# Optimization experiments

Hardware: AMD Instinct MI355X
Metric: run time of the kernel (lower is better)

The kernel has to match this reference:

```python
import jax, jax.numpy as jnp
import numpy as np

K = 20
EPS = 1e-5
NEG_SLOPE = 0.2


def _bn(x, gamma, beta, axes):
    # batch-norm in training mode (batch statistics), per-channel on last axis
    mean = jnp.mean(x, axis=axes, keepdims=True)
    var = jnp.var(x, axis=axes, keepdims=True)
    return gamma * (x - mean) * jax.lax.rsqrt(var + EPS) + beta


def _lrelu(x):
    return jnp.where(x >= 0, x, NEG_SLOPE * x)


def setup_inputs() -> dict:
    key = jax.random.key(0)
    ks = jax.random.split(key, 8)
    B, C, N = 8, 6, 4096

    def w(k_, shape):
        fan_in = shape[-1]
        return jax.random.normal(k_, shape, jnp.float32) / np.sqrt(fan_in)

    return {
        "x": jax.random.normal(ks[0], (B, C, N), jnp.float32),
        "conv1_w": w(ks[1], (64, 12)),
        "bn1_g": jnp.ones((64,), jnp.float32), "bn1_b": jnp.zeros((64,), jnp.float32),
        "conv2_w": w(ks[2], (128, 64)),
        "bn2_g": jnp.ones((128,), jnp.float32), "bn2_b": jnp.zeros((128,), jnp.float32),
        "conv3_w": w(ks[3], (1024, 128)),
        "bn3_g": jnp.ones((1024,), jnp.float32), "bn3_b": jnp.zeros((1024,), jnp.float32),
        "fc1_w": w(ks[4], (512, 1024)),
        "bn4_g": jnp.ones((512,), jnp.float32), "bn4_b": jnp.zeros((512,), jnp.float32),
        "fc2_w": w(ks[5], (256, 512)),
        "bn5_g": jnp.ones((256,), jnp.float32), "bn5_b": jnp.zeros((256,), jnp.float32),
        "fc3_w": w(ks[6], (9, 256)), "fc3_b": jnp.zeros((9,), jnp.float32),
        "fc4_w": w(ks[7], (3, 256)), "fc4_b": jnp.zeros((3,), jnp.float32),
    }


def _get_graph_feature(x, k):
    # x: [B, C, N] -> [B, N, k, 2C]
    B, C, N = x.shape
    xt = jnp.transpose(x, (0, 2, 1))                      # [B, N, C]
    xx = jnp.sum(xt * xt, axis=-1)                        # [B, N]
    inner = jnp.einsum('bnc,bmc->bnm', xt, xt)            # [B, N, N]
    pd = 2.0 * inner - xx[:, :, None] - xx[:, None, :]    # -||xi-xj||^2
    _, idx = jax.lax.top_k(pd, k)                         # [B, N, k]
    nbr = xt[jnp.arange(B)[:, None, None], idx]           # [B, N, k, C]
    center = jnp.broadcast_to(xt[:, :, None, :], nbr.shape)
    return jnp.concatenate([nbr - center, center], axis=-1)  # [B, N, k, 2C]


def reference(x, conv1_w, bn1_g, bn1_b, conv2_w, bn2_g, bn2_b,
              conv3_w, bn3_g, bn3_b, fc1_w, bn4_g, bn4_b,
              fc2_w, bn5_g, bn5_b, fc3_w, fc3_b, fc4_w, fc4_b):
    B = x.shape[0]
    feat = _get_graph_feature(x, K)                            # [B, N, k, 12]
    h = _lrelu(_bn(jnp.einsum('bnkc,oc->bnko', feat, conv1_w), bn1_g, bn1_b, (0, 1, 2)))
    h = _lrelu(_bn(jnp.einsum('bnkc,oc->bnko', h, conv2_w), bn2_g, bn2_b, (0, 1, 2)))
    h = jnp.max(h, axis=2)                                     # [B, N, 128] max over k
    h = _lrelu(_bn(jnp.einsum('bnc,oc->bno', h, conv3_w), bn3_g, bn3_b, (0, 1)))
    g = jnp.max(h, axis=1)                                     # [B, 1024] max over points
    g = _lrelu(_bn(g @ fc1_w.T, bn4_g, bn4_b, (0,)))           # [B, 512]
    g = _lrelu(_bn(g @ fc2_w.T, bn5_g, bn5_b, (0,)))           # [B, 256]
    bias = (g @ fc4_w.T + fc4_b)[:, None, :]                   # [B, 1, 3]
    matrix = jnp.eye(3, dtype=x.dtype) + (g @ fc3_w.T + fc3_b).reshape(B, 3, 3)
    xyz = jnp.transpose(x[:, :3, :], (0, 2, 1))                # [B, N, 3]
    out = jnp.einsum('bnc,bcd->bnd', xyz, matrix) + bias       # [B, N, 3]
    return jnp.transpose(out, (0, 2, 1))                       # [B, 3, N]
```

## Files before the change

kernel.cpp:

```cpp
#include <hip/hip_runtime.h>
#include <math.h>
#include <stddef.h>


static constexpr float EPS_ = 1e-5f;

__global__ __launch_bounds__(256) void k_prep(const float* __restrict__ x,
                                              float* __restrict__ xtp,
                                              const float* __restrict__ w2,
                                              float* __restrict__ w2t)
{
    int i = blockIdx.x*256 + threadIdx.x;
    int b = i >> 12, n = i & 4095;
    const float* xb = x + (size_t)b*6*4096 + n;
    float v0 = xb[0], v1 = xb[4096], v2 = xb[2*4096];
    float v3 = xb[3*4096], v4 = xb[4*4096], v5 = xb[5*4096];
    float xx = v0*v0 + v1*v1 + v2*v2 + v3*v3 + v4*v4 + v5*v5;
    float4* o = (float4*)(xtp + (size_t)i*8);
    o[0] = make_float4(v0, v1, v2, v3);
    o[1] = make_float4(v4, v5, xx, 0.f);
    if (blockIdx.x < 2){
        int e = blockIdx.x*256 + threadIdx.x;
        for (int q = e; q < 64*128; q += 512){
            int c = q >> 7, oo = q & 127;
            w2t[q] = w2[oo*64 + c];
        }
    }
}

__device__ __forceinline__ float pd_calc(const float4 a0, const float4 a1,
                                         const float4 q0, const float4 q1)
{
    float dot = a0.x*q0.x;
    dot = fmaf(a0.y, q0.y, dot);
    dot = fmaf(a0.z, q0.z, dot);
    dot = fmaf(a0.w, q0.w, dot);
    dot = fmaf(a1.x, q1.x, dot);
    dot = fmaf(a1.y, q1.y, dot);
    return fmaf(2.f, dot, -a1.z - q1.z);
}

__device__ __forceinline__ unsigned fkey_(float f){
    unsigned u = __float_as_uint(f);
    return (u & 0x80000000u) ? ~u : (u | 0x80000000u);
}
__device__ __forceinline__ float finv_(unsigned k){
    return (k & 0x80000000u) ? __uint_as_float(k & 0x7fffffffu)
                             : __uint_as_float(~k);
}

#define TK_CAP 384
__global__ __launch_bounds__(256) void k_topk(const float* __restrict__ xtp,
                                              int* __restrict__ idxout)
{
    __shared__ float maxs[8][256];
    __shared__ float candv[4][TK_CAP];
    __shared__ int   candi[4][TK_CAP];
    __shared__ float Ts[8];
    __shared__ unsigned ccnt[4], ocnt[4], nwork;
    __shared__ unsigned short work[1024];

    const int t = threadIdx.x;
    const int rowbase = blockIdx.x << 3;
    const int b = rowbase >> 12;
    const float* xb = xtp + ((size_t)b << 15);

    float4 c0[8], c1[8];
    #pragma unroll
    for (int c = 0; c < 8; c++){
        const float4* p = (const float4*)(xtp + (size_t)(rowbase + c)*8);
        c0[c] = p[0]; c1[c] = p[1];
    }

    float mx[8];
    #pragma unroll
    for (int c = 0; c < 8; c++) mx[c] = -INFINITY;
    {
        const float4* qp = (const float4*)(xb + (size_t)t*8);
        for (int i = 0; i < 16; i++){
            float4 q0 = qp[0], q1 = qp[1];
            #pragma unroll
            for (int c = 0; c < 8; c++)
                mx[c] = fmaxf(mx[c], pd_calc(c0[c], c1[c], q0, q1));
            qp += 512;
        }
    }
    #pragma unroll
    for (int c = 0; c < 8; c++) maxs[c][t] = mx[c];
    __syncthreads();

    const int w = t >> 6, lane = t & 63;
    for (int cc = w; cc < 8; cc += 4){
        unsigned k0 = fkey_(maxs[cc][lane]);
        unsigned k1 = fkey_(maxs[cc][64  + lane]);
        unsigned k2 = fkey_(maxs[cc][128 + lane]);
        unsigned k3 = fkey_(maxs[cc][192 + lane]);
        unsigned lo = 0u;
        for (int bit = 31; bit >= 0; bit--){
            unsigned cand = lo | (1u << bit);
            int cnt = __popcll(__ballot(k0 >= cand))
                    + __popcll(__ballot(k1 >= cand))
                    + __popcll(__ballot(k2 >= cand))
                    + __popcll(__ballot(k3 >= cand));
            if (cnt >= 20) lo = cand;
        }
        if (lane == 0) Ts[cc] = finv_(lo);
    }
    __syncthreads();

    for (int p = 0; p < 2; p++){
        const int cb = p << 2;
        if (t < 4){ ccnt[t] = 0u; ocnt[t] = 0u; }
        if (t == 0) nwork = 0u;
        __syncthreads();

        #pragma unroll
        for (int c = 0; c < 4; c++){
            if (mx[cb + c] >= Ts[cb + c]){
                unsigned pos = atomicAdd(&nwork, 1u);
                work[pos] = (unsigned short)((c << 8) | t);
            }
        }
        __syncthreads();

        {
            int total = (int)nwork << 4;
            for (int e = t; e < total; e += 256){
                int ct = work[e >> 4];
                int c = ct >> 8, src = ct & 255;
                int m = ((e & 15) << 8) | src;
                const float4* pp = (const float4*)(xb + (size_t)m*8);
                float4 q0 = pp[0], q1 = pp[1];
                float pd = pd_calc(c0[cb + c], c1[cb + c], q0, q1);
                if (pd >= Ts[cb + c]){
                    unsigned pos = atomicAdd(&ccnt[c], 1u);
                    if (pos < TK_CAP){ candv[c][pos] = pd; candi[c][pos] = m; }
                }
            }
        }
        __syncthreads();

        {
            int n = (int)min(ccnt[w], (unsigned)TK_CAP);
            unsigned key[6]; int id[6];
            #pragma unroll
            for (int j = 0; j < 6; j++){
                int pz = (j << 6) | lane;
                bool ok = pz < n;
                key[j] = ok ? fkey_(candv[w][pz]) : 0u;
                id[j]  = ok ? candi[w][pz] : 0x7fffffff;
            }
            unsigned C = 0u;
            for (int bit = 31; bit >= 0; bit--){
                unsigned cand = C | (1u << bit);
                int cnt = 0;
                #pragma unroll
                for (int j = 0; j < 6; j++)
                    cnt += __popcll(__ballot(key[j] >= cand));
                if (cnt >= 20) C = cand;
            }
            int m = 0, e = 0;
            #pragma unroll
            for (int j = 0; j < 6; j++){
                m += __popcll(__ballot(key[j] > C));
                e += __popcll(__ballot(key[j] == C));
            }
            int* outp = idxout + (size_t)(rowbase + cb + w)*20;
            #pragma unroll
            for (int j = 0; j < 6; j++){
                if (key[j] > C){
                    unsigned pos = atomicAdd(&ocnt[w], 1u);
                    outp[pos] = id[j];
                }
            }
            int need = 20 - m;
            if (e <= need){
                #pragma unroll
                for (int j = 0; j < 6; j++){
                    if (key[j] == C){
                        unsigned pos = atomicAdd(&ocnt[w], 1u);
                        outp[pos] = id[j];
                    }
                }
            } else {
                for (int r = 0; r < need; r++){
                    int loc = 0x7fffffff;
                    #pragma unroll
                    for (int j = 0; j < 6; j++)
                        if (key[j] == C && id[j] < loc) loc = id[j];
                    int g = loc;
                    #pragma unroll
                    for (int s = 1; s < 64; s <<= 1) g = min(g, __shfl_xor(g, s));
                    #pragma unroll
                    for (int j = 0; j < 6; j++){
                        if (key[j] == C && id[j] == g){
                            key[j] = 0u;
                            unsigned pos = atomicAdd(&ocnt[w], 1u);
                            outp[pos] = g;
                        }
                    }
                }
            }
        }
        __syncthreads();
    }
}

__global__ __launch_bounds__(256) void k_bn1stats(const float* __restrict__ xtp,
                                                  const int* __restrict__ idxb,
                                                  const float* __restrict__ w1,
                                                  float* __restrict__ bn1sum,
                                                  float* __restrict__ bn1sq)
{
    __shared__ float fT[320*12];
    __shared__ float red[2][4][64];
    const int t = threadIdx.x;
    const int rowbase = blockIdx.x << 4;
    const int b = rowbase >> 12;

    for (int s = t; s < 320; s += 256){
        int r = s / 20, k = s % 20;
        int grow = rowbase + r;
        int m = idxb[(size_t)grow*20 + k];
        const float4* pn = (const float4*)(xtp + (size_t)((b << 12) | m)*8);
        const float4* pc = (const float4*)(xtp + (size_t)grow*8);
        float4 n0 = pn[0], n1 = pn[1], c0 = pc[0], c1 = pc[1];
        float* f = fT + s*12;
        ((float4*)f)[0] = make_float4(n0.x-c0.x, n0.y-c0.y, n0.z-c0.z, n0.w-c0.w);
        ((float4*)f)[1] = make_float4(n1.x-c1.x, n1.y-c1.y, c0.x, c0.y);
        ((float4*)f)[2] = make_float4(c0.z, c0.w, c1.x, c1.y);
    }
    __syncthreads();
    const int o = t & 63, grp = t >> 6;
    float w[12];
    #pragma unroll
    for (int c = 0; c < 12; c++) w[c] = w1[o*12 + c];
    float sm = 0.f, sq = 0.f;
    for (int s = grp*80; s < grp*80 + 80; s++){
        const float* f = fT + s*12;
        float4 f0 = *(const float4*)(f);
        float4 fa = *(const float4*)(f + 4);
        float4 fb = *(const float4*)(f + 8);
        float h = w[0]*f0.x + w[1]*f0.y + w[2]*f0.z + w[3]*f0.w
                + w[4]*fa.x + w[5]*fa.y + w[6]*fa.z + w[7]*fa.w
                + w[8]*fb.x + w[9]*fb.y + w[10]*fb.z + w[11]*fb.w;
        sm += h; sq = fmaf(h, h, sq);
    }
    red[0][grp][o] = sm; red[1][grp][o] = sq;
    __syncthreads();
    if (t < 64){
        float a = red[0][0][t] + red[0][1][t] + red[0][2][t] + red[0][3][t];
        float c2 = red[1][0][t] + red[1][1][t] + red[1][2][t] + red[1][3][t];
        atomicAdd(bn1sum + t, a);
        atomicAdd(bn1sq + t, c2);
    }
}

__global__ __launch_bounds__(256, 2) void k_conv12(
    const float* __restrict__ xtp, const int* __restrict__ idxb,
    const float* __restrict__ w1, const float* __restrict__ w2t,
    const float* __restrict__ bn1sum, const float* __restrict__ bn1sq,
    const float* __restrict__ bn1g, const float* __restrict__ bn1b,
    float* __restrict__ h2max, float* __restrict__ bn2sum, float* __restrict__ bn2sq)
{
    __shared__ float f1s[160*64];
    __shared__ float w2u[16*516];
    const int t = threadIdx.x;
    const int rowbase = blockIdx.x << 3;
    const int b = rowbase >> 12;

    const int jch = t & 63;
    float wr[12];
    #pragma unroll
    for (int c = 0; c < 12; c++) wr[c] = w1[jch*12 + c];
    float s1, t1;
    {
        float mean = bn1sum[jch]*(1.f/655360.f);
        float var  = bn1sq[jch]*(1.f/655360.f) - mean*mean;
        s1 = bn1g[jch]/sqrtf(var + EPS_);
        t1 = bn1b[jch] - mean*s1;
    }

    float* fT = w2u;
    if (t < 160){
        int r = t / 20;
        int grow = rowbase + r;
        int m = idxb[(size_t)grow*20 + (t - r*20)];
        const float4* pn = (const float4*)(xtp + (size_t)((b << 12) | m)*8);
        const float4* pc = (const float4*)(xtp + (size_t)grow*8);
        float4 n0 = pn[0], n1 = pn[1], c0 = pc[0], c1 = pc[1];
        float* f = fT + t*12;
        ((float4*)f)[0] = make_float4(n0.x-c0.x, n0.y-c0.y, n0.z-c0.z, n0.w-c0.w);
        ((float4*)f)[1] = make_float4(n1.x-c1.x, n1.y-c1.y, c0.x, c0.y);
        ((float4*)f)[2] = make_float4(c0.z, c0.w, c1.x, c1.y);
    }
    __syncthreads();
    {
        for (int vid = t; vid < 10240; vid += 256){
            int vec = vid >> 6;
            const float* f = fT + vec*12;
            float4 f0 = *(const float4*)(f);
            float4 fa = *(const float4*)(f + 4);
            float4 fb = *(const float4*)(f + 8);
            float acc = wr[0]*f0.x + wr[1]*f0.y + wr[2]*f0.z + wr[3]*f0.w
                      + wr[4]*fa.x + wr[5]*fa.y + wr[6]*fa.z + wr[7]*fa.w
                      + wr[8]*fb.x + wr[9]*fb.y + wr[10]*fb.z + wr[11]*fb.w;
            float v = fmaf(s1, acc, t1);
            int key = (((vec >> 2) ^ vec) & 7) << 2;
            f1s[(vec << 6) + (jch ^ key)] = fmaxf(v, 0.2f*v);
        }
    }
    __syncthreads();
    {
        float4 tmp[8];
        #pragma unroll
        for (int i = 0; i < 8; i++) tmp[i] = ((const float4*)w2t)[t + (i << 8)];
        #pragma unroll
        for (int i = 0; i < 8; i++){
            int q = t + (i << 8);
            int jr = q >> 5, o4 = q & 31;
            *(float4*)&w2u[(o4 >> 1)*516 + (jr << 3) + ((o4 & 1) << 2)] = tmp[i];
        }
    }
    __syncthreads();

    const int vg = t & 15, og = t >> 4;
    const float* fp = f1s + vg*10*64;
    const float* wp = w2u + og*516;
    int kw[10];
    #pragma unroll
    for (int i = 0; i < 10; i++){
        int vec = vg*10 + i;
        kw[i] = (((vec >> 2) ^ vec) & 7) << 2;
    }

    float h[10][8];
    #pragma unroll
    for (int i = 0; i < 10; i++)
        #pragma unroll
        for (int oi = 0; oi < 8; oi++) h[i][oi] = 0.f;

    for (int jl = 0; jl < 64; jl += 4){
        float wv[4][8];
        #pragma unroll
        for (int jj = 0; jj < 4; jj++){
            *(float4*)&wv[jj][0] = *(const float4*)&wp[((jl + jj) << 3)];
            *(float4*)&wv[jj][4] = *(const float4*)&wp[((jl + jj) << 3) + 4];
        }
        #pragma unroll
        for (int i = 0; i < 10; i++){
            float fv[4];
            *(float4*)fv = *(const float4*)&fp[(i << 6) + (jl ^ kw[i])];
            #pragma unroll
            for (int jj = 0; jj < 4; jj++)
                #pragma unroll
                for (int oi = 0; oi < 8; oi++)
                    h[i][oi] = fmaf(fv[jj], wv[jj][oi], h[i][oi]);
        }
    }

    float mxl[8], sml[8], sql[8];
    #pragma unroll
    for (int oi = 0; oi < 8; oi++){
        float v = h[0][oi];
        mxl[oi] = v; sml[oi] = v; sql[oi] = v*v;
    }
    #pragma unroll
    for (int i = 1; i < 10; i++)
        #pragma unroll
        for (int oi = 0; oi < 8; oi++){
            float v = h[i][oi];
            mxl[oi] = fmaxf(mxl[oi], v);
            sml[oi] += v;
            sql[oi] = fmaf(v, v, sql[oi]);
        }
    __syncthreads();
    {
        int base = vg*132 + (og << 3);
        *(float4*)&w2u[base]        = *(float4*)&mxl[0];
        *(float4*)&w2u[base + 4]    = *(float4*)&mxl[4];
        *(float4*)&w2u[2112 + base]     = *(float4*)&sml[0];
        *(float4*)&w2u[2112 + base + 4] = *(float4*)&sml[4];
        *(float4*)&w2u[4224 + base]     = *(float4*)&sql[0];
        *(float4*)&w2u[4224 + base + 4] = *(float4*)&sql[4];
    }
    __syncthreads();
    for (int it = t; it < 1024; it += 256){
        int r = it >> 7, o = it & 127;
        float m = fmaxf(w2u[(r << 1)*132 + o],
                        w2u[((r << 1) | 1)*132 + o]);
        h2max[(size_t)(rowbase + r)*128 + o] = m;
    }
    if (t < 128){
        float s = 0.f, qq = 0.f;
        #pragma unroll
        for (int u = 0; u < 16; u++){
            s  += w2u[2112 + u*132 + t];
            qq += w2u[4224 + u*132 + t];
        }
        atomicAdd(bn2sum + t, s);
        atomicAdd(bn2sq + t, qq);
    }
}

__global__ __launch_bounds__(256) void k_wt3(const float* __restrict__ w3,
                                             float* __restrict__ w3t)
{
    int i = blockIdx.x*256 + threadIdx.x;
    int j = i >> 10, o = i & 1023;
    w3t[i] = w3[(size_t)o*128 + j];
}

__global__ __launch_bounds__(256, 2) void k_conv3(const float* __restrict__ h2max,
    const float* __restrict__ bn2sum, const float* __restrict__ bn2sq,
    const float* __restrict__ bn2g, const float* __restrict__ bn2b,
    const float* __restrict__ w3t,
    float* __restrict__ bn3sum, float* __restrict__ bn3sq, unsigned int* __restrict__ gkey)
{
    __shared__ float f2[64*132];
    __shared__ float w3s[8192];
    __shared__ float bn2stL[256];
    const int t = threadIdx.x;
    const int bid = blockIdx.x;
    const int idx = bid >> 3;
    const int rt = (bid & 7)*64 + (idx >> 4);
    const int ot = idx & 15;
    const int rowbase = rt << 6;
    const int obase = ot << 6;
    const int b = rowbase >> 12;

    if (t < 128){
        float mean = bn2sum[t]*(1.f/655360.f);
        float var  = bn2sq[t]*(1.f/655360.f) - mean*mean;
        float s = bn2g[t]/sqrtf(var + EPS_);
        bn2stL[t] = s;
        bn2stL[128 + t] = bn2b[t] - mean*s;
    }
    __syncthreads();

    for (int e = t; e < 64*128; e += 256){
        int r = e >> 7, c = e & 127;
        float v = h2max[(size_t)(rowbase + r)*128 + c];
        float u = fmaf(bn2stL[c], v, bn2stL[128 + c]);
        f2[r*132 + c] = fmaxf(u, 0.2f*u);
    }
    {
        float4 tmp[8];
        #pragma unroll
        for (int i = 0; i < 8; i++){
            int q = t + (i << 8);
            tmp[i] = *(const float4*)&w3t[(size_t)(q >> 4)*1024 + obase + ((q & 15) << 2)];
        }
        #pragma unroll
        for (int i = 0; i < 8; i++) ((float4*)w3s)[t + (i << 8)] = tmp[i];
    }
    __syncthreads();

    const int oq = t & 15, rg = t >> 4;
    const int o0 = oq << 2, r0 = rg << 2;
    float h[4][4];
    #pragma unroll
    for (int rr = 0; rr < 4; rr++)
        #pragma unroll
        for (int oi = 0; oi < 4; oi++) h[rr][oi] = 0.f;

    for (int jl = 0; jl < 128; jl += 4){
        float wv[4][4];
        #pragma unroll
        for (int jj = 0; jj < 4; jj++)
            *(float4*)wv[jj] = *(const float4*)&w3s[(jl + jj)*64 + o0];
        float fr[4][4];
        #pragma unroll
        for (int rr = 0; rr < 4; rr++)
            *(float4*)fr[rr] = *(const float4*)&f2[(r0 + rr)*132 + jl];
        #pragma unroll
        for (int jj = 0; jj < 4; jj++)
            #pragma unroll
            for (int rr = 0; rr < 4; rr++)
                #pragma unroll
                for (int oi = 0; oi < 4; oi++)
                    h[rr][oi] = fmaf(fr[rr][jj], wv[jj][oi], h[rr][oi]);
    }

    float sml[4], sql[4], mxl[4];
    #pragma unroll
    for (int oi = 0; oi < 4; oi++){
        float v = h[0][oi];
        sml[oi] = v; sql[oi] = v*v; mxl[oi] = v;
    }
    #pragma unroll
    for (int rr = 1; rr < 4; rr++)
        #pragma unroll
        for (int oi = 0; oi < 4; oi++){
            float v = h[rr][oi];
            sml[oi] += v;
            sql[oi] = fmaf(v, v, sql[oi]);
            mxl[oi] = fmaxf(mxl[oi], v);
        }
    __syncthreads();
    float* scr = f2;
    *(float4*)&scr[(rg << 6) + o0]        = *(float4*)&sml[0];
    *(float4*)&scr[1024 + (rg << 6) + o0] = *(float4*)&sql[0];
    *(float4*)&scr[2048 + (rg << 6) + o0] = *(float4*)&mxl[0];
    __syncthreads();
    if (t < 192){
        int stat = t >> 6, o = t & 63;
        if (stat == 0){
            float s = 0.f;
            #pragma unroll
            for (int g2 = 0; g2 < 16; g2++) s += scr[(g2 << 6) + o];
            atomicAdd(bn3sum + obase + o, s);
        } else if (stat == 1){
            float s = 0.f;
            #pragma unroll
            for (int g2 = 0; g2 < 16; g2++) s += scr[1024 + (g2 << 6) + o];
            atomicAdd(bn3sq + obase + o, s);
        } else {
            float m = scr[2048 + o];
            #pragma unroll
            for (int g2 = 1; g2 < 16; g2++) m = fmaxf(m, scr[2048 + (g2 << 6) + o]);
            unsigned u = __float_as_uint(m);
            unsigned key = (u & 0x80000000u) ? ~u : (u | 0x80000000u);
            atomicMax(gkey + (b << 10) + obase + o, key);
        }
    }
}

__global__ void k_bn3g(const float* __restrict__ sum, const float* __restrict__ sq,
                       const unsigned int* __restrict__ gkey,
                       const float* __restrict__ gamma, const float* __restrict__ beta,
                       float* __restrict__ g)
{
    int o = blockIdx.x*256 + threadIdx.x;
    if (o < 1024){
        float mean = sum[o]*(1.f/32768.f);
        float var  = sq[o]*(1.f/32768.f) - mean*mean;
        float s = gamma[o]/sqrtf(var + EPS_);
        float tt = beta[o] - mean*s;
        for (int b = 0; b < 8; b++){
            unsigned k = gkey[(b << 10) + o];
            unsigned u = (k & 0x80000000u) ? (k & 0x7fffffffu) : ~k;
            float v = __uint_as_float(u);
            float xv = fmaf(s, v, tt);
            g[(b << 10) + o] = fmaxf(xv, 0.2f*xv);
        }
    }
}

__global__ __launch_bounds__(256) void k_fc(const float* __restrict__ in,
                                            const float* __restrict__ w,
                                            float* __restrict__ out, int Kdim, int Odim)
{
    int wid = (blockIdx.x*256 + threadIdx.x) >> 6;
    int lane = threadIdx.x & 63;
    int nout = 8*Odim;
    if (wid >= nout) return;
    int b = wid / Odim, o = wid - b*Odim;
    const float* gi = in + (size_t)b*Kdim;
    const float* wr = w + (size_t)o*Kdim;
    float acc = 0.f;
    for (int c = lane; c < Kdim; c += 64) acc = fmaf(gi[c], wr[c], acc);
    #pragma unroll
    for (int s = 32; s > 0; s >>= 1) acc += __shfl_xor(acc, s);
    if (lane == 0) out[(size_t)b*Odim + o] = acc;
}

__global__ void k_bnb(const float* __restrict__ h, const float* __restrict__ gamma,
                      const float* __restrict__ beta, float* __restrict__ g, int C)
{
    int o = blockIdx.x*256 + threadIdx.x;
    if (o < C){
        float s = 0.f, q = 0.f;
        for (int b = 0; b < 8; b++){ float v = h[(size_t)b*C + o]; s += v; q = fmaf(v, v, q); }
        float mean = s*0.125f;
        float var  = q*0.125f - mean*mean;
        float sc = gamma[o]/sqrtf(var + EPS_);
        float tt = beta[o] - mean*sc;
        for (int b = 0; b < 8; b++){
            float xv = fmaf(sc, h[(size_t)b*C + o], tt);
            g[(size_t)b*C + o] = fmaxf(xv, 0.2f*xv);
        }
    }
}

__global__ void k_head(const float* __restrict__ g5,
                       const float* __restrict__ fc3w, const float* __restrict__ fc3b,
                       const float* __restrict__ fc4w, const float* __restrict__ fc4b,
                       float* __restrict__ mat, float* __restrict__ bias3)
{
    int t = threadIdx.x;
    if (t < 96){
        int b = t / 12, j = t % 12;
        const float* gi = g5 + b*256;
        if (j < 9){
            const float* w = fc3w + j*256;
            float a = fc3b[j];
            for (int c = 0; c < 256; c++) a = fmaf(gi[c], w[c], a);
            if (j == 0 || j == 4 || j == 8) a += 1.f;
            mat[b*9 + j] = a;
        } else {
            int d = j - 9;
            const float* w = fc4w + d*256;
            float a = fc4b[d];
            for (int c = 0; c < 256; c++) a = fmaf(gi[c], w[c], a);
            bias3[b*3 + d] = a;
        }
    }
}

__global__ __launch_bounds__(256) void k_out(const float* __restrict__ x,
                                             const float* __restrict__ mat,
                                             const float* __restrict__ bias3,
                                             float* __restrict__ out)
{
    int i = blockIdx.x*256 + threadIdx.x;
    int n = i & 4095, bd = i >> 12;
    int b = bd / 3, d = bd - b*3;
    const float* xb = x + (size_t)b*6*4096 + n;
    const float* M = mat + b*9;
    out[i] = xb[0]*M[d] + xb[4096]*M[3 + d] + xb[2*4096]*M[6 + d] + bias3[b*3 + d];
}

extern "C" void kernel_launch(void* const* d_in, const int* in_sizes, int n_in,
                              void* d_out, int out_size, void* d_ws, size_t ws_size,
                              hipStream_t stream)
{
    const float* x     = (const float*)d_in[0];
    const float* w1    = (const float*)d_in[1];
    const float* bn1g  = (const float*)d_in[2];
    const float* bn1b  = (const float*)d_in[3];
    const float* w2    = (const float*)d_in[4];
    const float* bn2g  = (const float*)d_in[5];
    const float* bn2b  = (const float*)d_in[6];
    const float* w3    = (const float*)d_in[7];
    const float* bn3gm = (const float*)d_in[8];
    const float* bn3bt = (const float*)d_in[9];
    const float* fc1w  = (const float*)d_in[10];
    const float* bn4g  = (const float*)d_in[11];
    const float* bn4b  = (const float*)d_in[12];
    const float* fc2w  = (const float*)d_in[13];
    const float* bn5g  = (const float*)d_in[14];
    const float* bn5b  = (const float*)d_in[15];
    const float* fc3w  = (const float*)d_in[16];
    const float* fc3b  = (const float*)d_in[17];
    const float* fc4w  = (const float*)d_in[18];
    const float* fc4b  = (const float*)d_in[19];
    float* out = (float*)d_out;

    char* ws = (char*)d_ws;
    float* xtp   = (float*)(ws);
    float* w3t_g = (float*)(ws);
    int*   idxb  = (int*)  (ws + 1048576);
    float* h2max = (float*)(ws + 3670016);
    float* zs    = (float*)(ws + 20447232);
    float* bn1sum = zs;            float* bn1sq = zs + 64;
    float* bn2sum = zs + 128;      float* bn2sq = zs + 256;
    float* bn3sum = zs + 384;      float* bn3sq = zs + 1408;
    unsigned int* gkey = (unsigned int*)(zs + 2432);
    float* tail  = (float*)(ws + 20489728);
    float* g     = tail;
    float* h4    = tail + 8192;
    float* g4    = tail + 12288;
    float* h5    = tail + 16384;
    float* g5    = tail + 18432;
    float* mat   = tail + 20480;
    float* bias3 = tail + 20552;
    float* w2t_g = (float*)(ws + 20573568);

    hipMemsetAsync(zs, 0, 42496, stream);

    k_prep    <<<128,   256, 0, stream>>>(x, xtp, w2, w2t_g);
    k_topk    <<<4096,  256, 0, stream>>>(xtp, idxb);
    k_bn1stats<<<2048,  256, 0, stream>>>(xtp, idxb, w1, bn1sum, bn1sq);
    k_conv12  <<<4096,  256, 0, stream>>>(xtp, idxb, w1, w2t_g,
                                          bn1sum, bn1sq, bn1g, bn1b,
                                          h2max, bn2sum, bn2sq);
    k_wt3     <<<512,   256, 0, stream>>>(w3, w3t_g);
    k_conv3   <<<8192,  256, 0, stream>>>(h2max, bn2sum, bn2sq, bn2g, bn2b,
                                          w3t_g, bn3sum, bn3sq, gkey);
    k_bn3g    <<<4,     256, 0, stream>>>(bn3sum, bn3sq, gkey, bn3gm, bn3bt, g);
    k_fc      <<<1024,  256, 0, stream>>>(g, fc1w, h4, 1024, 512);
    k_bnb     <<<2,     256, 0, stream>>>(h4, bn4g, bn4b, g4, 512);
    k_fc      <<<512,   256, 0, stream>>>(g4, fc2w, h5, 512, 256);
    k_bnb     <<<1,     256, 0, stream>>>(h5, bn5g, bn5b, g5, 256);
    k_head    <<<1,     128, 0, stream>>>(g5, fc3w, fc3b, fc4w, fc4b, mat, bias3);
    k_out     <<<384,   256, 0, stream>>>(x, mat, bias3, out);
}
```

Measured before the change: 648.8 us.

## Fuse FC tail into single-block kernel and hoist w2 loads in conv12

Replaces the chain of bn3/fc1/bn4/fc2/bn5/head kernels with one 1024-thread single-block kernel that keeps intermediates in shared memory, removing several kernel launches and global round trips. It also issues the w2t global loads at the start of k_conv12 so their latency overlaps earlier work. The fused tail computes the fully-connected layers on a single compute unit with per-thread row dot products, which limits bandwidth and parallelism for the 2 MB fc1 weight read.

Result: slower. 1.209 ms (+86.4%).

```diff
diff --git a/kernel.cpp b/kernel.cpp
--- a/kernel.cpp
+++ b/kernel.cpp
@@ -269,6 +269,10 @@
     const int rowbase = blockIdx.x << 3;
     const int b = rowbase >> 12;
 
+    float4 wst[8];
+    #pragma unroll
+    for (int i = 0; i < 8; i++) wst[i] = ((const float4*)w2t)[t + (i << 8)];
+
     const int jch = t & 63;
     float wr[12];
     #pragma unroll
@@ -312,14 +316,11 @@
     }
     __syncthreads();
     {
-        float4 tmp[8];
-        #pragma unroll
-        for (int i = 0; i < 8; i++) tmp[i] = ((const float4*)w2t)[t + (i << 8)];
         #pragma unroll
         for (int i = 0; i < 8; i++){
             int q = t + (i << 8);
             int jr = q >> 5, o4 = q & 31;
-            *(float4*)&w2u[(o4 >> 1)*516 + (jr << 3) + ((o4 & 1) << 2)] = tmp[i];
+            *(float4*)&w2u[(o4 >> 1)*516 + (jr << 3) + ((o4 & 1) << 2)] = wst[i];
         }
     }
     __syncthreads();
@@ -526,72 +527,100 @@
     }
 }
 
-__global__ void k_bn3g(const float* __restrict__ sum, const float* __restrict__ sq,
-                       const unsigned int* __restrict__ gkey,
-                       const float* __restrict__ gamma, const float* __restrict__ beta,
-                       float* __restrict__ g)
-{
-    int o = blockIdx.x*256 + threadIdx.x;
-    if (o < 1024){
-        float mean = sum[o]*(1.f/32768.f);
-        float var  = sq[o]*(1.f/32768.f) - mean*mean;
-        float s = gamma[o]/sqrtf(var + EPS_);
-        float tt = beta[o] - mean*s;
+__global__ __launch_bounds__(1024) void k_tail(
+    const float* __restrict__ bn3sum, const float* __restrict__ bn3sq,
+    const unsigned int* __restrict__ gkey,
+    const float* __restrict__ bn3gm, const float* __restrict__ bn3bt,
+    const float* __restrict__ fc1w, const float* __restrict__ bn4g,
+    const float* __restrict__ bn4b,
+    const float* __restrict__ fc2w, const float* __restrict__ bn5g,
+    const float* __restrict__ bn5b,
+    const float* __restrict__ fc3w, const float* __restrict__ fc3b,
+    const float* __restrict__ fc4w, const float* __restrict__ fc4b,
+    float* __restrict__ mat, float* __restrict__ bias3)
+{
+    __shared__ float gL[8*1024];
+    __shared__ float h4L[8*512];
+    __shared__ float g4L[8*512];
+    __shared__ float h5L[8*256];
+    __shared__ float g5L[8*256];
+    const int t = threadIdx.x;
+
+    {
+        float mean = bn3sum[t]*(1.f/32768.f);
+        float var  = bn3sq[t]*(1.f/32768.f) - mean*mean;
+        float s = bn3gm[t]/sqrtf(var + EPS_);
+        float tt = bn3bt[t] - mean*s;
         for (int b = 0; b < 8; b++){
-            unsigned k = gkey[(b << 10) + o];
+            unsigned k = gkey[(b << 10) + t];
             unsigned u = (k & 0x80000000u) ? (k & 0x7fffffffu) : ~k;
             float v = __uint_as_float(u);
             float xv = fmaf(s, v, tt);
-            g[(b << 10) + o] = fmaxf(xv, 0.2f*xv);
-        }
-    }
-}
-
-__global__ __launch_bounds__(256) void k_fc(const float* __restrict__ in,
-                                            const float* __restrict__ w,
-                                            float* __restrict__ out, int Kdim, int Odim)
-{
-    int wid = (blockIdx.x*256 + threadIdx.x) >> 6;
-    int lane = threadIdx.x & 63;
-    int nout = 8*Odim;
-    if (wid >= nout) return;
-    int b = wid / Odim, o = wid - b*Odim;
-    const float* gi = in + (size_t)b*Kdim;
-    const float* wr = w + (size_t)o*Kdim;
-    float acc = 0.f;
-    for (int c = lane; c < Kdim; c += 64) acc = fmaf(gi[c], wr[c], acc);
-    #pragma unroll
-    for (int s = 32; s > 0; s >>= 1) acc += __shfl_xor(acc, s);
-    if (lane == 0) out[(size_t)b*Odim + o] = acc;
-}
-
-__global__ void k_bnb(const float* __restrict__ h, const float* __restrict__ gamma,
-                      const float* __restrict__ beta, float* __restrict__ g, int C)
-{
-    int o = blockIdx.x*256 + threadIdx.x;
-    if (o < C){
+            gL[(b << 10) + t] = fmaxf(xv, 0.2f*xv);
+        }
+    }
+    __syncthreads();
+    for (int e = t; e < 4096; e += 1024){
+        int b = e >> 9, o = e & 511;
+        const float* gi = gL + (b << 10);
+        const float* wr = fc1w + (size_t)o*1024;
+        float acc = 0.f;
+        for (int c = 0; c < 1024; c += 4){
+            float4 wv = *(const float4*)&wr[c];
+            float4 gv = *(const float4*)&gi[c];
+            acc = fmaf(gv.x, wv.x, acc);
+            acc = fmaf(gv.y, wv.y, acc);
+            acc = fmaf(gv.z, wv.z, acc);
+            acc = fmaf(gv.w, wv.w, acc);
+        }
+        h4L[(b << 9) + o] = acc;
+    }
+    __syncthreads();
+    if (t < 512){
         float s = 0.f, q = 0.f;
-        for (int b = 0; b < 8; b++){ float v = h[(size_t)b*C + o]; s += v; q = fmaf(v, v, q); }
+        for (int b = 0; b < 8; b++){ float v = h4L[(b << 9) + t]; s += v; q = fmaf(v, v, q); }
         float mean = s*0.125f;
         float var  = q*0.125f - mean*mean;
-        float sc = gamma[o]/sqrtf(var + EPS_);
-        float tt = beta[o] - mean*sc;
+        float sc = bn4g[t]/sqrtf(var + EPS_);
+        float tt = bn4b[t] - mean*sc;
         for (int b = 0; b < 8; b++){
-            float xv = fmaf(sc, h[(size_t)b*C + o], tt);
-            g[(size_t)b*C + o] = fmaxf(xv, 0.2f*xv);
-        }
-    }
-}
-
-__global__ void k_head(const float* __restrict__ g5,
-                       const float* __restrict__ fc3w, const float* __restrict__ fc3b,
-                       const float* __restrict__ fc4w, const float* __restrict__ fc4b,
-                       float* __restrict__ mat, float* __restrict__ bias3)
-{
-    int t = threadIdx.x;
+            float xv = fmaf(sc, h4L[(b << 9) + t], tt);
+            g4L[(b << 9) + t] = fmaxf(xv, 0.2f*xv);
+        }
+    }
+    __syncthreads();
+    for (int e = t; e < 2048; e += 1024){
+        int b = e >> 8, o = e & 255;
+        const float* gi = g4L + (b << 9);
+        const float* wr = fc2w + (size_t)o*512;
+        float acc = 0.f;
+        for (int c = 0; c < 512; c += 4){
+            float4 wv = *(const float4*)&wr[c];
+            float4 gv = *(const float4*)&gi[c];
+            acc = fmaf(gv.x, wv.x, acc);
+            acc = fmaf(gv.y, wv.y, acc);
+            acc = fmaf(gv.z, wv.z, acc);
+            acc = fmaf(gv.w, wv.w, acc);
+        }
+        h5L[(b << 8) + o] = acc;
+    }
+    __syncthreads();
+    if (t < 256){
+        float s = 0.f, q = 0.f;
+        for (int b = 0; b < 8; b++){ float v = h5L[(b << 8) + t]; s += v; q = fmaf(v, v, q); }
+        float mean = s*0.125f;
+        float var  = q*0.125f - mean*mean;
+        float sc = bn5g[t]/sqrtf(var + EPS_);
+        float tt = bn5b[t] - mean*sc;
+        for (int b = 0; b < 8; b++){
+            float xv = fmaf(sc, h5L[(b << 8) + t], tt);
+            g5L[(b << 8) + t] = fmaxf(xv, 0.2f*xv);
+        }
+    }
+    __syncthreads();
     if (t < 96){
         int b = t / 12, j = t % 12;
-        const float* gi = g5 + b*256;
+        const float* gi = g5L + b*256;
         if (j < 9){
             const float* w = fc3w + j*256;
             float a = fc3b[j];
@@ -658,13 +687,8 @@
     float* bn3sum = zs + 384;      float* bn3sq = zs + 1408;
     unsigned int* gkey = (unsigned int*)(zs + 2432);
     float* tail  = (float*)(ws + 20489728);
-    float* g     = tail;
-    float* h4    = tail + 8192;
-    float* g4    = tail + 12288;
-    float* h5    = tail + 16384;
-    float* g5    = tail + 18432;
-    float* mat   = tail + 20480;
-    float* bias3 = tail + 20552;
+    float* mat   = tail;
+    float* bias3 = tail + 72;
     float* w2t_g = (float*)(ws + 20573568);
 
     hipMemsetAsync(zs, 0, 42496, stream);
@@ -678,11 +702,8 @@
     k_wt3     <<<512,   256, 0, stream>>>(w3, w3t_g);
     k_conv3   <<<8192,  256, 0, stream>>>(h2max, bn2sum, bn2sq, bn2g, bn2b,
                                           w3t_g, bn3sum, bn3sq, gkey);
-    k_bn3g    <<<4,     256, 0, stream>>>(bn3sum, bn3sq, gkey, bn3gm, bn3bt, g);
-    k_fc      <<<1024,  256, 0, stream>>>(g, fc1w, h4, 1024, 512);
-    k_bnb     <<<2,     256, 0, stream>>>(h4, bn4g, bn4b, g4, 512);
-    k_fc      <<<512,   256, 0, stream>>>(g4, fc2w, h5, 512, 256);
-    k_bnb     <<<1,     256, 0, stream>>>(h5, bn5g, bn5b, g5, 256);
-    k_head    <<<1,     128, 0, stream>>>(g5, fc3w, fc3b, fc4w, fc4b, mat, bias3);
+    k_tail    <<<1,    1024, 0, stream>>>(bn3sum, bn3sq, gkey, bn3gm, bn3bt,
+                                          fc1w, bn4g, bn4b, fc2w, bn5g, bn5b,
+                                          fc3w, fc3b, fc4w, fc4b, mat, bias3);
     k_out     <<<384,   256, 0, stream>>>(x, mat, bias3, out);
 }
```
